# Performance work log

Hardware: AMD Instinct MI355X
Metric: run time of the kernel (lower is better)

## Reference

```python
import jax, jax.numpy as jnp
import numpy as np

N_NODES = 100000


def _gcn_conv(x, W, b, src, dst, num_nodes):
    # x: [N, Fin] -> h: [N, Fout]
    h = x @ W
    # symmetric normalization deg^-1/2[src] * deg^-1/2[dst] (self-loops already appended)
    ones = jnp.ones(src.shape[0], dtype=x.dtype)
    deg = jax.ops.segment_sum(ones, dst, num_segments=num_nodes)
    dinv = jnp.where(deg > 0, jax.lax.rsqrt(deg), 0.0)
    norm = dinv[src] * dinv[dst]  # [E]
    msg = h[src] * norm[:, None]  # [E, Fout] -- dominant memory traffic
    out = jax.ops.segment_sum(msg, dst, num_segments=num_nodes)
    return out + b


def setup_inputs() -> dict:
    key = jax.random.key(0)
    ks = jax.random.split(key, 8)
    N, F_IN, H = N_NODES, 128, 64
    E = 3200000
    x = jax.random.normal(ks[0], (N, F_IN), dtype=jnp.float32)
    edge_index = jax.random.randint(ks[1], (2, E), 0, N, dtype=jnp.int64)
    s1 = 1.0 / np.sqrt(F_IN)
    s2 = 1.0 / np.sqrt(H)
    return {
        "x": x,
        "edge_index": edge_index,
        "W1": jax.random.normal(ks[2], (F_IN, H), dtype=jnp.float32) * s1,
        "b1": jnp.zeros((H,), dtype=jnp.float32),
        "W2": jax.random.normal(ks[3], (H, H), dtype=jnp.float32) * s2,
        "b2": jnp.zeros((H,), dtype=jnp.float32),
        "W_time": jax.random.normal(ks[4], (H, 1), dtype=jnp.float32) * s2,
        "b_time": jnp.zeros((1,), dtype=jnp.float32),
        "W_event": jax.random.normal(ks[5], (H, 1), dtype=jnp.float32) * s2,
        "b_event": jnp.zeros((1,), dtype=jnp.float32),
    }


def reference(x, edge_index, W1, b1, W2, b2, W_time, b_time, W_event, b_event):
    N = x.shape[0]
    # GCNConv default: add self-loops before normalization/aggregation
    loops = jnp.arange(N, dtype=edge_index.dtype)
    src = jnp.concatenate([edge_index[0], loops])
    dst = jnp.concatenate([edge_index[1], loops])

    h = jax.nn.relu(_gcn_conv(x, W1, b1, src, dst, N))
    # dropout is identity in eval mode
    h = jax.nn.relu(_gcn_conv(h, W2, b2, src, dst, N))

    survival_time = h @ W_time + b_time    # [N, 1]
    event_status = h @ W_event + b_event   # [N, 1]
    return survival_time, event_status
```

## Files before the change

kernel.cpp:

```cpp
#include <hip/hip_runtime.h>
#include <math.h>

constexpr int H = 64;
constexpr int FIN = 128;
constexpr int BIN_SHIFT = 8;
constexpr int BIN_NODES = 1 << BIN_SHIFT;
constexpr int MAX_BINS = 512;
constexpr int BIN_CAP = 10240;
constexpr int SRC_BITS = 24;
constexpr unsigned SRC_MASK = (1u << SRC_BITS) - 1;
constexpr int KB_TPB = 512;
constexpr int KB_BLOCKS = 512;
constexpr int KB_ITER = 13;

typedef __attribute__((ext_vector_type(8))) __bf16 bf16x8;
typedef __attribute__((ext_vector_type(4))) float f32x4;
typedef __attribute__((ext_vector_type(2))) float f32x2;

__device__ inline unsigned short f2bf(float f) {
    unsigned u = __builtin_bit_cast(unsigned, f);
    unsigned rnd = 0x7FFFu + ((u >> 16) & 1u);
    return (unsigned short)((u + rnd) >> 16);
}
__device__ inline float bflo(unsigned u) { return __builtin_bit_cast(float, u << 16); }
__device__ inline float bfhi(unsigned u) { return __builtin_bit_cast(float, u & 0xFFFF0000u); }

__device__ inline int wave_incl_scan(int v, int lane) {
#pragma unroll
    for (int off = 1; off < 64; off <<= 1) {
        int t = __shfl_up(v, off);
        if (lane >= off) v += t;
    }
    return v;
}

__global__ __launch_bounds__(512) void k_bin(
    const int* __restrict__ src, const int* __restrict__ dst, int E, int nbins,
    int* __restrict__ gcnt, int* __restrict__ binned) {
    __shared__ int hist[MAX_BINS];
    __shared__ int base[MAX_BINS];
    __shared__ int loff[MAX_BINS];
    __shared__ int words[KB_ITER * KB_TPB];
    __shared__ int wsum[8];
    int tid = threadIdx.x, lane = tid & 63, wid = tid >> 6;
    long long e0 = (long long)E * blockIdx.x / gridDim.x;
    long long e1 = (long long)E * (blockIdx.x + 1) / gridDim.x;
    int chunk = (int)(e1 - e0);
    for (int i = tid; i < MAX_BINS; i += KB_TPB) hist[i] = 0;
    __syncthreads();
    int packed[KB_ITER];
#pragma unroll
    for (int i = 0; i < KB_ITER; ++i) {
        int o = i * KB_TPB + tid;
        packed[i] = -1;
        if (o < chunk) {
            int d = dst[e0 + o];
            int b = d >> BIN_SHIFT;
            int r = atomicAdd(&hist[b], 1);
            packed[i] = (b << 22) | ((d & (BIN_NODES - 1)) << 14) | r;
        }
    }
    __syncthreads();
    {
        int c0 = hist[tid];
        int incl = wave_incl_scan(c0, lane);
        if (lane == 63) wsum[wid] = incl;
        __syncthreads();
        int woff = 0;
        for (int w = 0; w < wid; ++w) woff += wsum[w];
        loff[tid] = woff + incl - c0;
        if (tid < nbins && c0) base[tid] = tid * BIN_CAP + atomicAdd(&gcnt[tid], c0);
    }
    __syncthreads();
#pragma unroll
    for (int i = 0; i < KB_ITER; ++i) {
        int o = i * KB_TPB + tid;
        if (o < chunk) {
            unsigned w = (unsigned)packed[i];
            int b = (int)(w >> 22);
            int dl = (int)((w >> 14) & 0xFF);
            int r = (int)(w & 0x3FFF);
            words[loff[b] + r] = (int)(((unsigned)dl << SRC_BITS) | (unsigned)src[e0 + o]);
        }
    }
    __syncthreads();
    for (int b = tid; b < nbins; b += KB_TPB) {
        int n = hist[b];
        if (!n) continue;
        int g = base[b];
        int l = loff[b];
        int i = 0;
        while (i < n && ((g + i) & 3)) { binned[g + i] = words[l + i]; ++i; }
        for (; i + 4 <= n; i += 4) {
            int4 v = make_int4(words[l + i], words[l + i + 1], words[l + i + 2], words[l + i + 3]);
            *(int4*)&binned[g + i] = v;
        }
        for (; i < n; ++i) binned[g + i] = words[l + i];
    }
    for (int o = KB_ITER * KB_TPB + tid; o < chunk; o += KB_TPB) {
        int d = dst[e0 + o];
        int b = d >> BIN_SHIFT;
        int r = b * BIN_CAP + atomicAdd(&gcnt[b], 1);
        binned[r] = (int)(((unsigned)(d & (BIN_NODES - 1)) << SRC_BITS) | (unsigned)src[e0 + o]);
    }
}

__global__ __launch_bounds__(512) void k_binsort(
    const int* __restrict__ gcnt, const int* __restrict__ binned, int N, int E, int nbins,
    int* __restrict__ csr_src, int* __restrict__ rowptr, float* __restrict__ dinv) {
    __shared__ int binex[MAX_BINS];
    __shared__ int cnt[BIN_NODES];
    __shared__ int excl[BIN_NODES];
    __shared__ int rnk[BIN_NODES];
    __shared__ int wsum[8];
    int bin = blockIdx.x;
    int tid = threadIdx.x, lane = tid & 63, wid = tid >> 6;
    {
        int v = (tid < nbins) ? gcnt[tid] : 0;
        int incl = wave_incl_scan(v, lane);
        if (lane == 63) wsum[wid] = incl;
        __syncthreads();
        int woff = 0;
        for (int w = 0; w < wid; ++w) woff += wsum[w];
        binex[tid] = woff + incl - v;
    }
    if (tid < BIN_NODES) { cnt[tid] = 0; rnk[tid] = 0; }
    __syncthreads();
    int n = gcnt[bin];
    int gbase = binex[bin];
    const int* bp = binned + (size_t)bin * BIN_CAP;
    for (int i = tid; i < n; i += 512)
        atomicAdd(&cnt[((unsigned)bp[i]) >> SRC_BITS], 1);
    __syncthreads();
    int v = 0, incl = 0;
    if (tid < BIN_NODES) {
        v = cnt[tid];
        incl = wave_incl_scan(v, lane);
        if (lane == 63) wsum[wid] = incl;
    }
    __syncthreads();
    if (tid < BIN_NODES) {
        int woff = 0;
        for (int w = 0; w < wid; ++w) woff += wsum[w];
        int ex = woff + incl - v;
        excl[tid] = ex;
        int node = bin * BIN_NODES + tid;
        if (node < N) {
            rowptr[node] = gbase + ex;
            dinv[node] = 1.0f / sqrtf((float)v + 1.0f);
        }
    }
    if (bin == 0 && tid == 0) rowptr[N] = E;
    __syncthreads();
    for (int i = tid; i < n; i += 512) {
        unsigned w = (unsigned)bp[i];
        int dl = w >> SRC_BITS;
        int r = atomicAdd(&rnk[dl], 1);
        csr_src[gbase + excl[dl] + r] = (int)(w & SRC_MASK);
    }
}

template<int K, bool BF16_IN>
__global__ __launch_bounds__(256) void k_mgemm(
    const void* __restrict__ Xv, const float* __restrict__ W,
    const float* __restrict__ dinv, int N, unsigned short* __restrict__ A16) {
    constexpr int LDK = K + 8;
    __shared__ short sX[64 * LDK];
    __shared__ short sWt[64 * LDK];
    int tid = threadIdx.x;
    for (int idx = tid; idx < K * 64; idx += 256) {
        int k = idx >> 6, c = idx & 63;
        sWt[c * LDK + k] = (short)f2bf(W[idx]);
    }
    if constexpr (BF16_IN) {
        const unsigned short* Xs = (const unsigned short*)Xv;
        int row = tid >> 2, q0 = (tid & 3) * 16;
        int grow = blockIdx.x * 64 + row;
        uint4 u0 = make_uint4(0, 0, 0, 0), u1 = u0;
        if (grow < N) {
            const uint4* xp = (const uint4*)(Xs + (size_t)grow * K + q0);
            u0 = xp[0];
            u1 = xp[1];
        }
        uint4* dp = (uint4*)&sX[row * LDK + q0];
        dp[0] = u0;
        dp[1] = u1;
    } else {
        const float* X = (const float*)Xv;
        int row = tid >> 2;
        int q0 = (tid & 3) * (K / 4);
        int grow = blockIdx.x * 64 + row;
        const float* xp = X + (size_t)grow * K + q0;
        unsigned* dstp = (unsigned*)&sX[row * LDK + q0];
#pragma unroll
        for (int i = 0; i < K / 16; ++i) {
            float4 v = make_float4(0.f, 0.f, 0.f, 0.f);
            if (grow < N) v = *(const float4*)(xp + i * 4);
            unsigned lo = (unsigned)f2bf(v.x) | ((unsigned)f2bf(v.y) << 16);
            unsigned hi = (unsigned)f2bf(v.z) | ((unsigned)f2bf(v.w) << 16);
            dstp[i * 2] = lo;
            dstp[i * 2 + 1] = hi;
        }
    }
    __syncthreads();
    int w = tid >> 6, lane = tid & 63;
    int mrow = lane & 15, kgrp = lane >> 4;
    f32x4 acc[4] = {};
    const short* xbase = &sX[(16 * w + mrow) * LDK + kgrp * 8];
    const short* wbase = &sWt[mrow * LDK + kgrp * 8];
#pragma unroll
    for (int t = 0; t < K / 32; ++t) {
        bf16x8 a = *(const bf16x8*)(xbase + 32 * t);
#pragma unroll
        for (int c = 0; c < 4; ++c) {
            bf16x8 b = *(const bf16x8*)(wbase + 16 * c * LDK + 32 * t);
            acc[c] = __builtin_amdgcn_mfma_f32_16x16x32_bf16(a, b, acc[c], 0, 0, 0);
        }
    }
    int r0g = blockIdx.x * 64 + 16 * w + kgrp * 4;
#pragma unroll
    for (int r = 0; r < 4; ++r) {
        int rg = r0g + r;
        if (rg < N) {
            float dv = dinv[rg];
#pragma unroll
            for (int c = 0; c < 4; ++c)
                A16[(size_t)rg * H + 16 * c + mrow] = f2bf(acc[c][r] * dv);
        }
    }
}

__device__ inline void acc8(f32x2* acc, uint4 u) {
    f32x2 v0 = {bflo(u.x), bfhi(u.x)};
    f32x2 v1 = {bflo(u.y), bfhi(u.y)};
    f32x2 v2 = {bflo(u.z), bfhi(u.z)};
    f32x2 v3 = {bflo(u.w), bfhi(u.w)};
    acc[0] += v0; acc[1] += v1; acc[2] += v2; acc[3] += v3;
}

template<bool FUSE>
__global__ __launch_bounds__(256) void k_gather(
    const int* __restrict__ rowptr, const int* __restrict__ csr_src,
    const float* __restrict__ dinv, const unsigned short* __restrict__ A16,
    unsigned short* __restrict__ X2, int N,
    const float* __restrict__ bias, const float* __restrict__ Wt, const float* __restrict__ bt,
    const float* __restrict__ We, const float* __restrict__ be, float* __restrict__ out) {
    int w = threadIdx.x >> 6;
    int lane = threadIdx.x & 63;
    int grp = lane >> 3, sub = lane & 7;
    const uint4* A8 = (const uint4*)A16;
    int nodeA = blockIdx.x * 8 + w;
    int nodeB = nodeA + 4;
    int begA = 0, endA = 0, begB = 0, endB = 0;
    if (nodeA < N) { begA = rowptr[nodeA]; endA = rowptr[nodeA + 1]; }
    if (nodeB < N) { begB = rowptr[nodeB]; endB = rowptr[nodeB + 1]; }
    int mA0 = endA - begA; if (mA0 > 64) mA0 = 64;
    int mB0 = endB - begB; if (mB0 > 64) mB0 = 64;
    int idA = (lane < mA0) ? csr_src[begA + lane] : 0;
    int idB = (lane < mB0) ? csr_src[begB + lane] : 0;
    f32x2 aA[4] = {}, aB[4] = {};
    if (grp == 0 && nodeA < N) acc8(aA, A8[(size_t)nodeA * 8 + sub]);
    if (grp == 0 && nodeB < N) acc8(aB, A8[(size_t)nodeB * 8 + sub]);

    auto gather_node = [&](int beg, int end, int idFirst, f32x2* acc) {
        f32x2 t[4] = {};
        for (int e0 = beg; e0 < end; e0 += 64) {
            int m = end - e0; if (m > 64) m = 64;
            int id = (e0 == beg) ? idFirst : ((lane < m) ? csr_src[e0 + lane] : 0);
            int c = 0;
            for (; c + 16 <= m; c += 16) {
                int s0 = __shfl(id, c + grp);
                int s1 = __shfl(id, c + 8 + grp);
                uint4 u0 = A8[(size_t)s0 * 8 + sub];
                uint4 u1 = A8[(size_t)s1 * 8 + sub];
                acc8(acc, u0);
                acc8(t, u1);
            }
            for (; c < m; c += 8) {
                int cc = c + grp;
                int s = __shfl(id, cc < m ? cc : 0);
                if (cc < m) acc8(acc, A8[(size_t)s * 8 + sub]);
            }
        }
#pragma unroll
        for (int j = 0; j < 4; ++j) acc[j] += t[j];
    };
    gather_node(begA, endA, idA, aA);
    gather_node(begB, endB, idB, aB);

#pragma unroll
    for (int off = 8; off < 64; off <<= 1) {
#pragma unroll
        for (int j = 0; j < 4; ++j) {
            aA[j][0] += __shfl_xor(aA[j][0], off);
            aA[j][1] += __shfl_xor(aA[j][1], off);
            aB[j][0] += __shfl_xor(aB[j][0], off);
            aB[j][1] += __shfl_xor(aB[j][1], off);
        }
    }
    if (grp == 0) {
#pragma unroll
        for (int which = 0; which < 2; ++which) {
            int node = which ? nodeB : nodeA;
            if (node >= N) continue;
            f32x2* a = which ? aB : aA;
            float dv = dinv[node];
            float r[8];
#pragma unroll
            for (int j = 0; j < 4; ++j) { r[2 * j] = a[j][0] * dv; r[2 * j + 1] = a[j][1] * dv; }
            int f = sub * 8;
            if (!FUSE) {
                unsigned short o[8];
#pragma unroll
                for (int j = 0; j < 8; ++j) o[j] = f2bf(fmaxf(r[j] + bias[f + j], 0.f));
                *(uint4*)(X2 + (size_t)node * H + f) = *(uint4*)o;
            } else {
                float p1 = 0.f, p2 = 0.f;
#pragma unroll
                for (int j = 0; j < 8; ++j) {
                    float g = fmaxf(r[j] + bias[f + j], 0.f);
                    p1 += g * Wt[f + j];
                    p2 += g * We[f + j];
                }
#pragma unroll
                for (int off = 1; off < 8; off <<= 1) {
                    p1 += __shfl_xor(p1, off);
                    p2 += __shfl_xor(p2, off);
                }
                if (sub == 0) {
                    out[node] = p1 + bt[0];
                    out[N + node] = p2 + be[0];
                }
            }
        }
    }
}

extern "C" void kernel_launch(void* const* d_in, const int* in_sizes, int n_in,
                              void* d_out, int out_size, void* d_ws, size_t ws_size,
                              hipStream_t stream) {
    const float* x  = (const float*)d_in[0];
    const int* edge = (const int*)d_in[1];
    const float* W1 = (const float*)d_in[2];
    const float* b1 = (const float*)d_in[3];
    const float* W2 = (const float*)d_in[4];
    const float* b2 = (const float*)d_in[5];
    const float* Wt = (const float*)d_in[6];
    const float* bt = (const float*)d_in[7];
    const float* We = (const float*)d_in[8];
    const float* be = (const float*)d_in[9];

    int N = in_sizes[0] / FIN;
    int E = in_sizes[1] / 2;
    const int* src = edge;
    const int* dst = edge + E;
    int nbins = (N + BIN_NODES - 1) >> BIN_SHIFT;

    char* ws = (char*)d_ws;
    size_t off = 0;
    auto alloc = [&](size_t bytes) {
        void* p = ws + off;
        off += (bytes + 255) & ~size_t(255);
        return p;
    };
    float* dinv    = (float*)alloc((size_t)N * sizeof(float));
    int*   rowptr  = (int*)alloc((size_t)(N + 1) * sizeof(int));
    int*   gcnt    = (int*)alloc((size_t)nbins * sizeof(int));
    int*   binned  = (int*)alloc((size_t)nbins * BIN_CAP * sizeof(int));
    int*   csr_src = (int*)alloc((size_t)E * sizeof(int));
    unsigned short* A16 = (unsigned short*)alloc((size_t)N * H * sizeof(unsigned short));
    unsigned short* X2  = (unsigned short*)alloc((size_t)N * H * sizeof(unsigned short));

    hipMemsetAsync(gcnt, 0, (size_t)nbins * sizeof(int), stream);
    k_bin<<<KB_BLOCKS, KB_TPB, 0, stream>>>(src, dst, E, nbins, gcnt, binned);
    k_binsort<<<nbins, 512, 0, stream>>>(gcnt, binned, N, E, nbins, csr_src, rowptr, dinv);

    int ggrid = (N + 63) / 64;
    k_mgemm<FIN, false><<<ggrid, 256, 0, stream>>>(x, W1, dinv, N, A16);
    k_gather<false><<<(N + 7) / 8, 256, 0, stream>>>(rowptr, csr_src, dinv, A16, X2, N,
                                                     b1, nullptr, nullptr, nullptr, nullptr, nullptr);

    k_mgemm<H, true><<<ggrid, 256, 0, stream>>>(X2, W2, dinv, N, A16);
    k_gather<true><<<(N + 7) / 8, 256, 0, stream>>>(rowptr, csr_src, dinv, A16, nullptr, N,
                                                    b2, Wt, bt, We, be, (float*)d_out);
}
```

Before: 217.1 us.

## Split feature dimension into two 32-wide halves with separate gather passes

The GEMM now writes its bf16 output into two separate 32-feature arrays, and each aggregation runs as two gather launches, one per half, combining the fused head outputs through a small float2 workspace. The aim is to halve the gathered table size per pass (6.4MB each) so it fits better in cache, raising the hit rate for random neighbour reads. The cost is reading the CSR indices twice and launching extra kernels, and each gather now fetches 64-byte rows, a smaller transaction per edge.

After: 302.7 us. +39.5%, slower.

```diff
diff --git a/kernel.cpp b/kernel.cpp
--- a/kernel.cpp
+++ b/kernel.cpp
@@ -163,7 +163,8 @@
 template<int K, bool BF16_IN>
 __global__ __launch_bounds__(256) void k_mgemm(
     const void* __restrict__ Xv, const float* __restrict__ W,
-    const float* __restrict__ dinv, int N, unsigned short* __restrict__ A16) {
+    const float* __restrict__ dinv, int N,
+    unsigned short* __restrict__ A16a, unsigned short* __restrict__ A16b) {
     constexpr int LDK = K + 8;
     __shared__ short sX[64 * LDK];
     __shared__ short sWt[64 * LDK];
@@ -224,8 +225,11 @@
         if (rg < N) {
             float dv = dinv[rg];
 #pragma unroll
-            for (int c = 0; c < 4; ++c)
-                A16[(size_t)rg * H + 16 * c + mrow] = f2bf(acc[c][r] * dv);
+            for (int c = 0; c < 4; ++c) {
+                unsigned short val = f2bf(acc[c][r] * dv);
+                if (c < 2) A16a[(size_t)rg * 32 + 16 * c + mrow] = val;
+                else       A16b[(size_t)rg * 32 + 16 * (c - 2) + mrow] = val;
+            }
         }
     }
 }
@@ -238,17 +242,18 @@
     acc[0] += v0; acc[1] += v1; acc[2] += v2; acc[3] += v3;
 }
 
-template<bool FUSE>
+template<int HALF, bool FUSE>
 __global__ __launch_bounds__(256) void k_gather(
     const int* __restrict__ rowptr, const int* __restrict__ csr_src,
-    const float* __restrict__ dinv, const unsigned short* __restrict__ A16,
-    unsigned short* __restrict__ X2, int N,
-    const float* __restrict__ bias, const float* __restrict__ Wt, const float* __restrict__ bt,
-    const float* __restrict__ We, const float* __restrict__ be, float* __restrict__ out) {
+    const float* __restrict__ dinv, const unsigned short* __restrict__ A16h,
+    unsigned short* __restrict__ X2h, int N,
+    const float* __restrict__ biash, const float* __restrict__ Wth, const float* __restrict__ bt,
+    const float* __restrict__ Weh, const float* __restrict__ be,
+    float2* __restrict__ hws, float* __restrict__ out) {
     int w = threadIdx.x >> 6;
     int lane = threadIdx.x & 63;
-    int grp = lane >> 3, sub = lane & 7;
-    const uint4* A8 = (const uint4*)A16;
+    int grp = lane >> 2, sub = lane & 3;
+    const uint4* A4 = (const uint4*)A16h;
     int nodeA = blockIdx.x * 8 + w;
     int nodeB = nodeA + 4;
     int begA = 0, endA = 0, begB = 0, endB = 0;
@@ -259,8 +264,8 @@
     int idA = (lane < mA0) ? csr_src[begA + lane] : 0;
     int idB = (lane < mB0) ? csr_src[begB + lane] : 0;
     f32x2 aA[4] = {}, aB[4] = {};
-    if (grp == 0 && nodeA < N) acc8(aA, A8[(size_t)nodeA * 8 + sub]);
-    if (grp == 0 && nodeB < N) acc8(aB, A8[(size_t)nodeB * 8 + sub]);
+    if (grp == 0 && nodeA < N) acc8(aA, A4[(size_t)nodeA * 4 + sub]);
+    if (grp == 0 && nodeB < N) acc8(aB, A4[(size_t)nodeB * 4 + sub]);
 
     auto gather_node = [&](int beg, int end, int idFirst, f32x2* acc) {
         f32x2 t[4] = {};
@@ -268,18 +273,18 @@
             int m = end - e0; if (m > 64) m = 64;
             int id = (e0 == beg) ? idFirst : ((lane < m) ? csr_src[e0 + lane] : 0);
             int c = 0;
-            for (; c + 16 <= m; c += 16) {
+            for (; c + 32 <= m; c += 32) {
                 int s0 = __shfl(id, c + grp);
-                int s1 = __shfl(id, c + 8 + grp);
-                uint4 u0 = A8[(size_t)s0 * 8 + sub];
-                uint4 u1 = A8[(size_t)s1 * 8 + sub];
+                int s1 = __shfl(id, c + 16 + grp);
+                uint4 u0 = A4[(size_t)s0 * 4 + sub];
+                uint4 u1 = A4[(size_t)s1 * 4 + sub];
                 acc8(acc, u0);
                 acc8(t, u1);
             }
-            for (; c < m; c += 8) {
+            for (; c < m; c += 16) {
                 int cc = c + grp;
                 int s = __shfl(id, cc < m ? cc : 0);
-                if (cc < m) acc8(acc, A8[(size_t)s * 8 + sub]);
+                if (cc < m) acc8(acc, A4[(size_t)s * 4 + sub]);
             }
         }
 #pragma unroll
@@ -289,7 +294,7 @@
     gather_node(begB, endB, idB, aB);
 
 #pragma unroll
-    for (int off = 8; off < 64; off <<= 1) {
+    for (int off = 4; off < 64; off <<= 1) {
 #pragma unroll
         for (int j = 0; j < 4; ++j) {
             aA[j][0] += __shfl_xor(aA[j][0], off);
@@ -312,24 +317,26 @@
             if (!FUSE) {
                 unsigned short o[8];
 #pragma unroll
-                for (int j = 0; j < 8; ++j) o[j] = f2bf(fmaxf(r[j] + bias[f + j], 0.f));
-                *(uint4*)(X2 + (size_t)node * H + f) = *(uint4*)o;
+                for (int j = 0; j < 8; ++j) o[j] = f2bf(fmaxf(r[j] + biash[f + j], 0.f));
+                *(uint4*)(X2h + (size_t)node * H + f) = *(uint4*)o;
             } else {
                 float p1 = 0.f, p2 = 0.f;
 #pragma unroll
                 for (int j = 0; j < 8; ++j) {
-                    float g = fmaxf(r[j] + bias[f + j], 0.f);
-                    p1 += g * Wt[f + j];
-                    p2 += g * We[f + j];
+                    float g = fmaxf(r[j] + biash[f + j], 0.f);
+                    p1 += g * Wth[f + j];
+                    p2 += g * Weh[f + j];
                 }
-#pragma unroll
-                for (int off = 1; off < 8; off <<= 1) {
-                    p1 += __shfl_xor(p1, off);
-                    p2 += __shfl_xor(p2, off);
-                }
+                p1 += __shfl_xor(p1, 1); p2 += __shfl_xor(p2, 1);
+                p1 += __shfl_xor(p1, 2); p2 += __shfl_xor(p2, 2);
                 if (sub == 0) {
-                    out[node] = p1 + bt[0];
-                    out[N + node] = p2 + be[0];
+                    if (HALF == 0) {
+                        hws[node] = make_float2(p1, p2);
+                    } else {
+                        float2 h = hws[node];
+                        out[node] = h.x + p1 + bt[0];
+                        out[N + node] = h.y + p2 + be[0];
+                    }
                 }
             }
         }
@@ -368,19 +375,26 @@
     int*   gcnt    = (int*)alloc((size_t)nbins * sizeof(int));
     int*   binned  = (int*)alloc((size_t)nbins * BIN_CAP * sizeof(int));
     int*   csr_src = (int*)alloc((size_t)E * sizeof(int));
-    unsigned short* A16 = (unsigned short*)alloc((size_t)N * H * sizeof(unsigned short));
-    unsigned short* X2  = (unsigned short*)alloc((size_t)N * H * sizeof(unsigned short));
+    unsigned short* A16a = (unsigned short*)alloc((size_t)N * 32 * sizeof(unsigned short));
+    unsigned short* A16b = (unsigned short*)alloc((size_t)N * 32 * sizeof(unsigned short));
+    unsigned short* X2   = (unsigned short*)alloc((size_t)N * H * sizeof(unsigned short));
+    float2* hws    = (float2*)alloc((size_t)N * sizeof(float2));
 
     hipMemsetAsync(gcnt, 0, (size_t)nbins * sizeof(int), stream);
     k_bin<<<KB_BLOCKS, KB_TPB, 0, stream>>>(src, dst, E, nbins, gcnt, binned);
     k_binsort<<<nbins, 512, 0, stream>>>(gcnt, binned, N, E, nbins, csr_src, rowptr, dinv);
 
     int ggrid = (N + 63) / 64;
-    k_mgemm<FIN, false><<<ggrid, 256, 0, stream>>>(x, W1, dinv, N, A16);
-    k_gather<false><<<(N + 7) / 8, 256, 0, stream>>>(rowptr, csr_src, dinv, A16, X2, N,
-                                                     b1, nullptr, nullptr, nullptr, nullptr, nullptr);
-
-    k_mgemm<H, true><<<ggrid, 256, 0, stream>>>(X2, W2, dinv, N, A16);
-    k_gather<true><<<(N + 7) / 8, 256, 0, stream>>>(rowptr, csr_src, dinv, A16, nullptr, N,
-                                                    b2, Wt, bt, We, be, (float*)d_out);
-}
+    int grid8 = (N + 7) / 8;
+    k_mgemm<FIN, false><<<ggrid, 256, 0, stream>>>(x, W1, dinv, N, A16a, A16b);
+    k_gather<0, false><<<grid8, 256, 0, stream>>>(rowptr, csr_src, dinv, A16a, X2, N,
+                                                  b1, nullptr, nullptr, nullptr, nullptr, nullptr, nullptr);
+    k_gather<1, false><<<grid8, 256, 0, stream>>>(rowptr, csr_src, dinv, A16b, X2 + 32, N,
+                                                  b1 + 32, nullptr, nullptr, nullptr, nullptr, nullptr, nullptr);
+
+    k_mgemm<H, true><<<ggrid, 256, 0, stream>>>(X2, W2, dinv, N, A16a, A16b);
+    k_gather<0, true><<<grid8, 256, 0, stream>>>(rowptr, csr_src, dinv, A16a, nullptr, N,
+                                                 b2, Wt, bt, We, be, hws, (float*)d_out);
+    k_gather<1, true><<<grid8, 256, 0, stream>>>(rowptr, csr_src, dinv, A16b, nullptr, N,
+                                                 b2 + 32, Wt + 32, bt, We + 32, be, hws, (float*)d_out);
+}
```
